# Kernel tuning notes

Hardware: AMD Instinct MI355X
Metric: run time of the kernel (lower is better)

The kernel has to match this reference:

```python
import jax, jax.numpy as jnp
import numpy as np

NUM_HEADS = 8
GROUPS = 8
EPS = 1e-5


def setup_inputs() -> dict:
    key = jax.random.key(0)
    ks = jax.random.split(key, 5)
    B, C, H, W = 2, 512, 64, 64
    x = jax.random.normal(ks[0], (B, C, H, W), dtype=jnp.float32)
    gn_w = jnp.ones((C,), dtype=jnp.float32)
    gn_b = jnp.zeros((C,), dtype=jnp.float32)
    qkv_w = jax.random.normal(ks[1], (3 * C, C), dtype=jnp.float32) * 0.02  # 1x1 conv weight
    qkv_b = jnp.zeros((3 * C,), dtype=jnp.float32)
    proj_w = jax.random.normal(ks[2], (C, C), dtype=jnp.float32) * 0.02
    proj_b = jnp.zeros((C,), dtype=jnp.float32)
    return {"x": x, "gn_w": gn_w, "gn_b": gn_b, "qkv_w": qkv_w,
            "qkv_b": qkv_b, "proj_w": proj_w, "proj_b": proj_b}


def group_norm(x, w, b):
    B, C, H, W = x.shape
    xg = x.reshape(B, GROUPS, C // GROUPS, H, W)
    mean = xg.mean(axis=(2, 3, 4), keepdims=True)
    var = xg.var(axis=(2, 3, 4), keepdims=True)  # biased, matching torch GroupNorm
    h = ((xg - mean) * jax.lax.rsqrt(var + EPS)).reshape(B, C, H, W)
    return h * w[None, :, None, None] + b[None, :, None, None]


def reference(x, gn_w, gn_b, qkv_w, qkv_b, proj_w, proj_b):
    B, C, H, W = x.shape
    nh = NUM_HEADS
    dh = C // nh
    scale = dh ** -0.5
    S = H * W

    h = group_norm(x, gn_w, gn_b)
    # 1x1 conv == per-pixel linear: (B,3C,H,W)
    qkv = jnp.einsum('bchw,oc->bohw', h, qkv_w) + qkv_b[None, :, None, None]
    qkv = qkv.reshape(B, 3, nh, dh, S)
    q = jnp.swapaxes(qkv[:, 0], -1, -2)  # (B, nh, S, dh)
    k = jnp.swapaxes(qkv[:, 1], -1, -2)
    v = jnp.swapaxes(qkv[:, 2], -1, -2)

    attn = jax.nn.softmax(jnp.einsum('bhsd,btd->bhst', q, k.reshape(B * nh, S, dh).reshape(B, nh, S, dh)) * scale, axis=-1) if False else jax.nn.softmax(jnp.einsum('bhsd,bhtd->bhst', q, k) * scale, axis=-1)
    out = jnp.einsum('bhst,bhtd->bhsd', attn, v)  # (B, nh, S, dh)
    out = jnp.swapaxes(out, -1, -2).reshape(B, C, H, W)
    out = jnp.einsum('bchw,oc->bohw', out, proj_w) + proj_b[None, :, None, None]
    return x + out
```

## Files before the change

### kernel.cpp

```cpp
#include <hip/hip_runtime.h>
#include <hip/hip_bf16.h>

typedef __attribute__((ext_vector_type(4)))  float  f32x4;
typedef __attribute__((ext_vector_type(16))) float  f32x16;
typedef __attribute__((ext_vector_type(8)))  short  s16x8;
typedef __attribute__((ext_vector_type(4)))  short  s16x4;
typedef __attribute__((ext_vector_type(4)))  unsigned u32x4;
typedef __attribute__((ext_vector_type(2)))  unsigned u32x2;

__device__ __forceinline__ float bf2f(short v) {
    unsigned u = ((unsigned)(unsigned short)v) << 16;
    return __builtin_bit_cast(float, u);
}
__device__ __forceinline__ short f2bf(float f) {
    unsigned u = __builtin_bit_cast(unsigned, f);
    u += 0x7fff + ((u >> 16) & 1);
    return (short)(u >> 16);
}
__device__ __forceinline__ unsigned cvt_pk_bf16(float lo, float hi) {
    unsigned r;
    asm("v_cvt_pk_bf16_f32 %0, %1, %2" : "=v"(r) : "v"(lo), "v"(hi));
    return r;
}
__device__ __forceinline__ float exp2_asm(float x) {
    float r; asm("v_exp_f32 %0, %1" : "=v"(r) : "v"(x)); return r;
}
__device__ __forceinline__ float log2_asm(float x) {
    float r; asm("v_log_f32 %0, %1" : "=v"(r) : "v"(x)); return r;
}
__device__ __forceinline__ void perm32swap(unsigned &a, unsigned &b) {
    u32x2 r = __builtin_amdgcn_permlane32_swap(a, b, false, false);
    a = r[0]; b = r[1];
}
__device__ __forceinline__ void gload16(const short* g, short* l) {
    __builtin_amdgcn_global_load_lds(
        (const __attribute__((address_space(1))) void*)g,
        (__attribute__((address_space(3))) void*)l, 16, 0, 0);
}

#define BATCH 2
#define CCH   512
#define SSP   4096
#define NH    8
#define DH    64

__global__ __launch_bounds__(256) void wcast_kernel(
    const float* __restrict__ qw, const float* __restrict__ pw,
    short* __restrict__ dq, short* __restrict__ dp)
{
    int idx = (blockIdx.x * 256 + threadIdx.x) * 8;
    const float* src; short* dst;
    if (idx < 786432) { src = qw + idx; dst = dq + idx; }
    else              { src = pw + (idx - 786432); dst = dp + (idx - 786432); }
    f32x4 a = *(const f32x4*)src;
    f32x4 b = *(const f32x4*)(src + 4);
    s16x8 o;
    o[0]=f2bf(a[0]); o[1]=f2bf(a[1]); o[2]=f2bf(a[2]); o[3]=f2bf(a[3]);
    o[4]=f2bf(b[0]); o[5]=f2bf(b[1]); o[6]=f2bf(b[2]); o[7]=f2bf(b[3]);
    *(s16x8*)dst = o;
}

__global__ __launch_bounds__(256) void gn_partial_kernel(
    const float* __restrict__ x, float* __restrict__ part)
{
    int bg = blockIdx.x >> 5, chunk = blockIdx.x & 31;
    const float* base = x + (size_t)bg * 262144 + chunk * 8192;
    int t = threadIdx.x, lane = t & 63, wave = t >> 6;
    float s = 0.f, ss = 0.f;
    #pragma unroll
    for (int k = 0; k < 8; ++k) {
        f32x4 v = *(const f32x4*)&base[k * 1024 + t * 4];
        #pragma unroll
        for (int j = 0; j < 4; ++j) { s += v[j]; ss += v[j] * v[j]; }
    }
    #pragma unroll
    for (int mask = 1; mask < 64; mask <<= 1) {
        s  += __shfl_xor(s,  mask);
        ss += __shfl_xor(ss, mask);
    }
    __shared__ float rs[4], rss[4];
    if (lane == 0) { rs[wave] = s; rss[wave] = ss; }
    __syncthreads();
    if (t == 0) {
        part[blockIdx.x * 2]     = rs[0] + rs[1] + rs[2] + rs[3];
        part[blockIdx.x * 2 + 1] = rss[0] + rss[1] + rss[2] + rss[3];
    }
}

__global__ void gn_final_kernel(const float* __restrict__ part, float* __restrict__ stats)
{
    int t = threadIdx.x;
    if (t < 16) {
        float s = 0.f, ss = 0.f;
        for (int c = 0; c < 32; ++c) {
            s  += part[(t * 32 + c) * 2];
            ss += part[(t * 32 + c) * 2 + 1];
        }
        float mean = s * (1.f / 262144.f);
        float var  = ss * (1.f / 262144.f) - mean * mean;
        stats[t * 2]     = mean;
        stats[t * 2 + 1] = rsqrtf(var + 1e-5f);
    }
}

__global__ __launch_bounds__(256) void gn_apply_kernel(
    const float* __restrict__ x, const float* __restrict__ gw, const float* __restrict__ gb,
    const float* __restrict__ stats, short* __restrict__ hbuf)
{
    __shared__ float tile[64][65];
    int id = blockIdx.x;
    int st = id & 63, ct = (id >> 6) & 7, b = id >> 9;
    int t  = threadIdx.x;
    float mean = stats[(b * 8 + ct) * 2], rstd = stats[(b * 8 + ct) * 2 + 1];
    #pragma unroll
    for (int pass = 0; pass < 4; ++pass) {
        int cr = pass * 16 + (t >> 4);
        int c  = ct * 64 + cr;
        f32x4 v = *(const f32x4*)&x[((size_t)(b * CCH + c)) * SSP + st * 64 + (t & 15) * 4];
        float w  = gw[c] * rstd;
        float bb = gb[c] - mean * w;
        #pragma unroll
        for (int j = 0; j < 4; ++j) tile[cr][(t & 15) * 4 + j] = v[j] * w + bb;
    }
    __syncthreads();
    int sr = t >> 2, cc0 = (t & 3) * 16;
    s16x8 o0, o1;
    #pragma unroll
    for (int j = 0; j < 8; ++j) {
        o0[j] = f2bf(tile[cc0 + j][sr]);
        o1[j] = f2bf(tile[cc0 + 8 + j][sr]);
    }
    short* dst = &hbuf[(size_t)(b * SSP + st * 64 + sr) * CCH + ct * 64 + cc0];
    *(s16x8*)dst = o0;
    *(s16x8*)(dst + 8) = o1;
}

template<int EPI>
__global__ __launch_bounds__(256) void gemm_bt_kernel(
    const short* __restrict__ A, const short* __restrict__ Bt,
    const float* __restrict__ bias,
    short* __restrict__ qout, short* __restrict__ kout, short* __restrict__ vout,
    const float* __restrict__ xres, float* __restrict__ out,
    int K)
{
    __shared__ short As[4096], Bs[4096];
    const int t = threadIdx.x;
    const int lane = t & 63, wave = t >> 6;
    const int wm = wave >> 1, wn = wave & 1;
    const int m0 = blockIdx.x * 128, n0 = blockIdx.y * 128;
    const int l15 = lane & 15, lq = lane >> 4;

    f32x4 acc[4][4];
    #pragma unroll
    for (int i = 0; i < 4; ++i)
        #pragma unroll
        for (int j = 0; j < 4; ++j) acc[i][j] = (f32x4){0.f, 0.f, 0.f, 0.f};

    for (int kk = 0; kk < K; kk += 32) {
        __syncthreads();
        #pragma unroll
        for (int i = 0; i < 2; ++i) {
            int idx = i * 256 + t;
            int row = idx >> 2, cb = idx & 3;
            int dst = ((row >> 4) << 9) + ((((row & 15)) | (cb << 4)) << 3);
            *(s16x8*)&As[dst] = *(const s16x8*)&A [(size_t)(m0 + row) * K + kk + cb * 8];
            *(s16x8*)&Bs[dst] = *(const s16x8*)&Bt[(size_t)(n0 + row) * K + kk + cb * 8];
        }
        __syncthreads();
        s16x8 af[4], bfr[4];
        #pragma unroll
        for (int mt = 0; mt < 4; ++mt) af[mt]  = *(const s16x8*)&As[(((wm * 4 + mt) << 9) + lane * 8)];
        #pragma unroll
        for (int nt = 0; nt < 4; ++nt) bfr[nt] = *(const s16x8*)&Bs[(((wn * 4 + nt) << 9) + lane * 8)];
        #pragma unroll
        for (int mt = 0; mt < 4; ++mt)
            #pragma unroll
            for (int nt = 0; nt < 4; ++nt)
                acc[mt][nt] = __builtin_amdgcn_mfma_f32_16x16x32_bf16(af[mt], bfr[nt], acc[mt][nt], 0, 0, 0);
    }

    #pragma unroll
    for (int mt = 0; mt < 4; ++mt) {
        const int r0 = m0 + wm * 64 + mt * 16 + lq * 4;
        #pragma unroll
        for (int nt = 0; nt < 4; ++nt) {
            const int c = n0 + wn * 64 + nt * 16 + l15;
            float bv = bias[c];
            if (EPI == 0) {
                int bb = r0 >> 12, tloc = r0 & 4095;
                if (c < 512) {
                    #pragma unroll
                    for (int i = 0; i < 4; ++i)
                        qout[(size_t)(r0 + i) * 512 + c] = f2bf(acc[mt][nt][i] + bv);
                } else if (c < 1024) {
                    int hh = (c - 512) >> 6, d = (c - 512) & 63;
                    int T = tloc >> 6, tb = (tloc >> 5) & 1;
                    size_t base = (((size_t)(bb * 8 + hh) * 64 + T) * 8 + tb * 4 + (d >> 4)) * 512
                                  + 256 * ((d >> 3) & 1) + (d & 7);
                    #pragma unroll
                    for (int i = 0; i < 4; ++i)
                        kout[base + ((tloc & 31) + i) * 8] = f2bf(acc[mt][nt][i] + bv);
                } else {
                    int hh = (c - 1024) >> 6, d = (c - 1024) & 63;
                    int T = tloc >> 6, s = (tloc >> 4) & 3, thi = (tloc >> 3) & 1, j0 = tloc & 7;
                    size_t base = (((size_t)(bb * 8 + hh) * 64 + T) * 8 + (d >> 5) * 4 + s) * 512
                                  + ((d & 31) + 32 * thi) * 8 + j0;
                    s16x4 pv;
                    #pragma unroll
                    for (int i = 0; i < 4; ++i) pv[i] = f2bf(acc[mt][nt][i] + bv);
                    *(s16x4*)&vout[base] = pv;
                }
            } else {
                int bb = r0 >> 12, s = r0 & 4095;
                size_t xi = (size_t)(bb * CCH + c) * SSP + s;
                f32x4 xv = *(const f32x4*)&xres[xi];
                f32x4 o  = xv + acc[mt][nt] + bv;
                *(f32x4*)&out[xi] = o;
            }
        }
    }
}

__global__ __launch_bounds__(256, 4) void attn_kernel(
    const short* __restrict__ qbuf, const short* __restrict__ kfrag,
    const short* __restrict__ vfrag,
    short* __restrict__ p0, short* __restrict__ p1, float* __restrict__ aout)
{
    __shared__ short Ks[2][4096];
    __shared__ short Vs[2][4096];
    const int t = threadIdx.x, lane = t & 63, wave = t >> 6;
    const int yy = blockIdx.y, bh = yy & 15, half = yy >> 4;
    const int b = bh >> 3, h = bh & 7;
    const int q0w = blockIdx.x * 128 + wave * 32;
    const int l31 = lane & 31, lh = lane >> 5;
    const int kv0 = half * 2048;

    s16x8 qf[4];
    {
        const short* qp = qbuf + (size_t)(b * SSP + q0w + l31) * 512 + h * 64 + 8 * lh;
        #pragma unroll
        for (int s = 0; s < 4; ++s) {
            s16x8 raw = *(const s16x8*)(qp + 16 * s);
            #pragma unroll
            for (int j = 0; j < 8; ++j) qf[s][j] = f2bf(bf2f(raw[j]) * 0.18033688011112042f);
        }
    }

    const short* kbase = kfrag + (size_t)bh * 262144 + lane * 8;
    const short* vbase = vfrag + (size_t)bh * 262144 + lane * 8;

    f32x16 oacc[2];
    oacc[0] = (f32x16){}; oacc[1] = (f32x16){};
    float m_ = -__builtin_inff(), l_ = 0.f;

    {
        const short* kg = kbase + (size_t)(kv0 >> 6) * 4096 + wave * 1024;
        gload16(kg,       &Ks[0][wave * 1024]);
        gload16(kg + 512, &Ks[0][wave * 1024 + 512]);
        const short* vg = vbase + (size_t)(kv0 >> 6) * 4096 + wave * 1024;
        gload16(vg,       &Vs[0][wave * 1024]);
        gload16(vg + 512, &Vs[0][wave * 1024 + 512]);
    }
    asm volatile("s_waitcnt vmcnt(0)" ::: "memory");
    __syncthreads();

    int cur = 0;
    for (int t0 = kv0; t0 < kv0 + 2048; t0 += 64) {
        if (t0 + 64 < kv0 + 2048) {
            int nb = cur ^ 1;
            const short* kg = kbase + (size_t)((t0 + 64) >> 6) * 4096 + wave * 1024;
            gload16(kg,       &Ks[nb][wave * 1024]);
            gload16(kg + 512, &Ks[nb][wave * 1024 + 512]);
            const short* vg = vbase + (size_t)((t0 + 64) >> 6) * 4096 + wave * 1024;
            gload16(vg,       &Vs[nb][wave * 1024]);
            gload16(vg + 512, &Vs[nb][wave * 1024 + 512]);
        }

        f32x16 sacc[2];
        sacc[0] = (f32x16){}; sacc[1] = (f32x16){};
        __builtin_amdgcn_s_setprio(1);
        #pragma unroll
        for (int s = 0; s < 4; ++s) {
            s16x8 k0 = *(const s16x8*)&Ks[cur][(0 + s) * 512 + lane * 8];
            s16x8 k1 = *(const s16x8*)&Ks[cur][(4 + s) * 512 + lane * 8];
            sacc[0] = __builtin_amdgcn_mfma_f32_32x32x16_bf16(k0, qf[s], sacc[0], 0, 0, 0);
            sacc[1] = __builtin_amdgcn_mfma_f32_32x32x16_bf16(k1, qf[s], sacc[1], 0, 0, 0);
        }
        __builtin_amdgcn_s_setprio(0);

        float mx = sacc[0][0];
        #pragma unroll
        for (int r = 1; r < 16; ++r) mx = fmaxf(mx, sacc[0][r]);
        #pragma unroll
        for (int r = 0; r < 16; ++r) mx = fmaxf(mx, sacc[1][r]);
        int calm = __all(mx <= m_ + 11.5f);
        if (!calm) {
            float g = fmaxf(mx, __shfl_xor(mx, 32));
            float mn = fmaxf(m_, g);
            float corr = exp2_asm(m_ - mn);
            m_ = mn;
            #pragma unroll
            for (int r = 0; r < 16; ++r) { oacc[0][r] *= corr; oacc[1][r] *= corr; }
            l_ *= corr;
        }
        float ts = 0.f;
        #pragma unroll
        for (int tb = 0; tb < 2; ++tb)
            #pragma unroll
            for (int r = 0; r < 16; ++r) {
                float e = exp2_asm(sacc[tb][r] - m_);
                sacc[tb][r] = e;
                ts += e;
            }
        ts += __shfl_xor(ts, 32);
        l_ += ts;

        unsigned w[16];
        #pragma unroll
        for (int tb = 0; tb < 2; ++tb)
            #pragma unroll
            for (int r = 0; r < 8; ++r)
                w[tb * 8 + r] = cvt_pk_bf16(sacc[tb][2 * r], sacc[tb][2 * r + 1]);
        #pragma unroll
        for (int s = 0; s < 4; ++s) {
            perm32swap(w[s * 4 + 0], w[s * 4 + 2]);
            perm32swap(w[s * 4 + 1], w[s * 4 + 3]);
        }

        __builtin_amdgcn_s_setprio(1);
        #pragma unroll
        for (int s = 0; s < 4; ++s) {
            u32x4 pb = { w[s * 4 + 0], w[s * 4 + 1], w[s * 4 + 2], w[s * 4 + 3] };
            s16x8 pB = __builtin_bit_cast(s16x8, pb);
            s16x8 v0 = *(const s16x8*)&Vs[cur][(0 + s) * 512 + lane * 8];
            s16x8 v1 = *(const s16x8*)&Vs[cur][(4 + s) * 512 + lane * 8];
            oacc[0] = __builtin_amdgcn_mfma_f32_32x32x16_bf16(v0, pB, oacc[0], 0, 0, 0);
            oacc[1] = __builtin_amdgcn_mfma_f32_32x32x16_bf16(v1, pB, oacc[1], 0, 0, 0);
        }
        __builtin_amdgcn_s_setprio(0);

        asm volatile("s_waitcnt vmcnt(0)" ::: "memory");
        __syncthreads();
        cur ^= 1;
    }

    short* pO = half ? p1 : p0;
    float linv = 1.f / l_;
    int q = q0w + l31;
    size_t obase = ((size_t)bh * 4096 + q) * 64;
    #pragma unroll
    for (int db = 0; db < 2; ++db)
        #pragma unroll
        for (int g = 0; g < 4; ++g) {
            s16x4 o;
            #pragma unroll
            for (int i = 0; i < 4; ++i) o[i] = f2bf(oacc[db][g * 4 + i] * linv);
            *(s16x4*)&pO[obase + db * 32 + g * 8 + lh * 4] = o;
        }
    if (lh == 0)
        aout[half * 65536 + bh * 4096 + q] = m_ + log2_asm(l_);
}

__global__ __launch_bounds__(256) void combine_kernel(
    const short* __restrict__ p0, const short* __restrict__ p1,
    const float* __restrict__ aout, short* __restrict__ ao)
{
    int bh = blockIdx.x >> 7, q = (blockIdx.x & 127) * 32 + (threadIdx.x >> 3);
    int d0 = (threadIdx.x & 7) * 8;
    size_t pi = ((size_t)bh * 4096 + q) * 64 + d0;
    s16x8 o1 = *(const s16x8*)&p0[pi];
    s16x8 o2 = *(const s16x8*)&p1[pi];
    float a1 = aout[bh * 4096 + q], a2 = aout[65536 + bh * 4096 + q];
    float M = fmaxf(a1, a2);
    float w1 = exp2_asm(a1 - M), w2 = exp2_asm(a2 - M);
    float inv = 1.f / (w1 + w2);
    w1 *= inv; w2 *= inv;
    s16x8 o;
    #pragma unroll
    for (int j = 0; j < 8; ++j) o[j] = f2bf(bf2f(o1[j]) * w1 + bf2f(o2[j]) * w2);
    int b = bh >> 3, h = bh & 7;
    *(s16x8*)&ao[(size_t)(b * SSP + q) * 512 + h * 64 + d0] = o;
}

extern "C" void kernel_launch(void* const* d_in, const int* in_sizes, int n_in,
                              void* d_out, int out_size, void* d_ws, size_t ws_size,
                              hipStream_t stream)
{
    (void)in_sizes; (void)n_in; (void)out_size; (void)ws_size;
    const float* x      = (const float*)d_in[0];
    const float* gn_w   = (const float*)d_in[1];
    const float* gn_b   = (const float*)d_in[2];
    const float* qkv_w  = (const float*)d_in[3];
    const float* qkv_b  = (const float*)d_in[4];
    const float* proj_w = (const float*)d_in[5];
    const float* proj_b = (const float*)d_in[6];
    float* out = (float*)d_out;
    char* ws = (char*)d_ws;

    short* hbuf  = (short*)(ws + 0);
    short* qbuf  = (short*)(ws + 8388608);
    short* kfrag = (short*)(ws + 16777216);
    short* vfrag = (short*)(ws + 25165824);
    short* aobuf = (short*)(ws + 33554432);
    short* wqkv  = (short*)(ws + 41943040);
    short* wproj = (short*)(ws + 43515904);
    float* part  = (float*)(ws + 44040192);
    float* stats = (float*)(ws + 44044288);
    float* ascal = (float*)(ws + 41943040);

    wcast_kernel<<<512, 256, 0, stream>>>(qkv_w, proj_w, wqkv, wproj);
    gn_partial_kernel<<<512, 256, 0, stream>>>(x, part);
    gn_final_kernel<<<1, 64, 0, stream>>>(part, stats);
    gn_apply_kernel<<<1024, 256, 0, stream>>>(x, gn_w, gn_b, stats, hbuf);
    gemm_bt_kernel<0><<<dim3(64, 12), 256, 0, stream>>>(hbuf, wqkv, qkv_b,
                                                        qbuf, kfrag, vfrag, nullptr, nullptr, 512);
    attn_kernel<<<dim3(32, 32), 256, 0, stream>>>(qbuf, kfrag, vfrag,
                                                  hbuf, aobuf, ascal);
    combine_kernel<<<2048, 256, 0, stream>>>(hbuf, aobuf, ascal, kfrag);
    gemm_bt_kernel<1><<<dim3(64, 4), 256, 0, stream>>>(kfrag, wproj, proj_b,
                                                       nullptr, nullptr, nullptr, x, out, 512);
}
```

Before: 158.7 us.

## Double-buffer GEMM tiles via async LDS loads and restructure attention softmax bookkeeping

The GEMM kernel now double-buffers its A/B tiles with global_load_lds, prefetching the next K slice while MFMAs run on the current one. This replaces the synchronous register-staged load followed by two barriers per step. In the attention kernel, the running max is folded into the score accumulator's initial value (nm). The row max uses v_max3 chains, and the row sum is computed by an extra MFMA against a ones vector instead of VALU adds and a shuffle. This trades extra MFMA work and a more intricate numerical path (bf16-rounded probabilities summed, with the max offset baked into the accumulators) for fewer VALU ops and better load/compute overlap.

```diff
diff --git a/kernel.cpp b/kernel.cpp
--- a/kernel.cpp
+++ b/kernel.cpp
@@ -27,6 +27,10 @@
 }
 __device__ __forceinline__ float log2_asm(float x) {
     float r; asm("v_log_f32 %0, %1" : "=v"(r) : "v"(x)); return r;
+}
+__device__ __forceinline__ float max3f(float a, float b, float c) {
+    float r; asm("v_max3_f32 %0, %1, %2, %3" : "=v"(r) : "v"(a), "v"(b), "v"(c));
+    return r;
 }
 __device__ __forceinline__ void perm32swap(unsigned &a, unsigned &b) {
     u32x2 r = __builtin_amdgcn_permlane32_swap(a, b, false, false);
@@ -143,40 +147,57 @@
     const float* __restrict__ xres, float* __restrict__ out,
     int K)
 {
-    __shared__ short As[4096], Bs[4096];
+    __shared__ short As[2][4096], Bs[2][4096];
     const int t = threadIdx.x;
     const int lane = t & 63, wave = t >> 6;
     const int wm = wave >> 1, wn = wave & 1;
     const int m0 = blockIdx.x * 128, n0 = blockIdx.y * 128;
     const int l15 = lane & 15, lq = lane >> 4;
 
+    const int s0r = ((t >> 6) << 4) | (t & 15),          s0c = (t >> 4) & 3;
+    const int s1r = (((256 + t) >> 6) << 4) | (t & 15),  s1c = (t >> 4) & 3;
+    const short* ga0 = A  + (size_t)(m0 + s0r) * K + s0c * 8;
+    const short* ga1 = A  + (size_t)(m0 + s1r) * K + s1c * 8;
+    const short* gb0 = Bt + (size_t)(n0 + s0r) * K + s0c * 8;
+    const short* gb1 = Bt + (size_t)(n0 + s1r) * K + s1c * 8;
+    const int wofs0 = wave * 512;
+    const int wofs1 = 2048 + wave * 512;
+
     f32x4 acc[4][4];
     #pragma unroll
     for (int i = 0; i < 4; ++i)
         #pragma unroll
         for (int j = 0; j < 4; ++j) acc[i][j] = (f32x4){0.f, 0.f, 0.f, 0.f};
 
+    gload16(ga0, &As[0][wofs0]);
+    gload16(ga1, &As[0][wofs1]);
+    gload16(gb0, &Bs[0][wofs0]);
+    gload16(gb1, &Bs[0][wofs1]);
+    asm volatile("s_waitcnt vmcnt(0)" ::: "memory");
+    __syncthreads();
+
+    int cur = 0;
     for (int kk = 0; kk < K; kk += 32) {
-        __syncthreads();
-        #pragma unroll
-        for (int i = 0; i < 2; ++i) {
-            int idx = i * 256 + t;
-            int row = idx >> 2, cb = idx & 3;
-            int dst = ((row >> 4) << 9) + ((((row & 15)) | (cb << 4)) << 3);
-            *(s16x8*)&As[dst] = *(const s16x8*)&A [(size_t)(m0 + row) * K + kk + cb * 8];
-            *(s16x8*)&Bs[dst] = *(const s16x8*)&Bt[(size_t)(n0 + row) * K + kk + cb * 8];
-        }
-        __syncthreads();
+        int nxt = cur ^ 1;
+        if (kk + 32 < K) {
+            gload16(ga0 + kk + 32, &As[nxt][wofs0]);
+            gload16(ga1 + kk + 32, &As[nxt][wofs1]);
+            gload16(gb0 + kk + 32, &Bs[nxt][wofs0]);
+            gload16(gb1 + kk + 32, &Bs[nxt][wofs1]);
+        }
         s16x8 af[4], bfr[4];
         #pragma unroll
-        for (int mt = 0; mt < 4; ++mt) af[mt]  = *(const s16x8*)&As[(((wm * 4 + mt) << 9) + lane * 8)];
-        #pragma unroll
-        for (int nt = 0; nt < 4; ++nt) bfr[nt] = *(const s16x8*)&Bs[(((wn * 4 + nt) << 9) + lane * 8)];
+        for (int mt = 0; mt < 4; ++mt) af[mt]  = *(const s16x8*)&As[cur][((wm * 4 + mt) << 9) + lane * 8];
+        #pragma unroll
+        for (int nt = 0; nt < 4; ++nt) bfr[nt] = *(const s16x8*)&Bs[cur][((wn * 4 + nt) << 9) + lane * 8];
         #pragma unroll
         for (int mt = 0; mt < 4; ++mt)
             #pragma unroll
             for (int nt = 0; nt < 4; ++nt)
                 acc[mt][nt] = __builtin_amdgcn_mfma_f32_16x16x32_bf16(af[mt], bfr[nt], acc[mt][nt], 0, 0, 0);
+        asm volatile("s_waitcnt vmcnt(0)" ::: "memory");
+        __syncthreads();
+        cur = nxt;
     }
 
     #pragma unroll
@@ -251,7 +272,12 @@
 
     f32x16 oacc[2];
     oacc[0] = (f32x16){}; oacc[1] = (f32x16){};
-    float m_ = -__builtin_inff(), l_ = 0.f;
+    f32x16 lacc = (f32x16){};
+    float nm = 0.f;
+
+    s16x8 ones;
+    #pragma unroll
+    for (int j = 0; j < 8; ++j) ones[j] = (short)0x3F80;
 
     {
         const short* kg = kbase + (size_t)(kv0 >> 6) * 4096 + wave * 1024;
@@ -276,51 +302,57 @@
             gload16(vg + 512, &Vs[nb][wave * 1024 + 512]);
         }
 
-        f32x16 sacc[2];
-        sacc[0] = (f32x16){}; sacc[1] = (f32x16){};
+        f32x16 sacc0, sacc1;
+        #pragma unroll
+        for (int r = 0; r < 16; ++r) { sacc0[r] = nm; sacc1[r] = nm; }
         __builtin_amdgcn_s_setprio(1);
         #pragma unroll
         for (int s = 0; s < 4; ++s) {
             s16x8 k0 = *(const s16x8*)&Ks[cur][(0 + s) * 512 + lane * 8];
             s16x8 k1 = *(const s16x8*)&Ks[cur][(4 + s) * 512 + lane * 8];
-            sacc[0] = __builtin_amdgcn_mfma_f32_32x32x16_bf16(k0, qf[s], sacc[0], 0, 0, 0);
-            sacc[1] = __builtin_amdgcn_mfma_f32_32x32x16_bf16(k1, qf[s], sacc[1], 0, 0, 0);
+            sacc0 = __builtin_amdgcn_mfma_f32_32x32x16_bf16(k0, qf[s], sacc0, 0, 0, 0);
+            sacc1 = __builtin_amdgcn_mfma_f32_32x32x16_bf16(k1, qf[s], sacc1, 0, 0, 0);
         }
         __builtin_amdgcn_s_setprio(0);
 
-        float mx = sacc[0][0];
-        #pragma unroll
-        for (int r = 1; r < 16; ++r) mx = fmaxf(mx, sacc[0][r]);
-        #pragma unroll
-        for (int r = 0; r < 16; ++r) mx = fmaxf(mx, sacc[1][r]);
-        int calm = __all(mx <= m_ + 11.5f);
+        float u0 = max3f(sacc0[0],  sacc0[1],  sacc0[2]);
+        float u1 = max3f(sacc0[3],  sacc0[4],  sacc0[5]);
+        float u2 = max3f(sacc0[6],  sacc0[7],  sacc0[8]);
+        float u3 = max3f(sacc0[9],  sacc0[10], sacc0[11]);
+        float u4 = max3f(sacc0[12], sacc0[13], sacc0[14]);
+        float u5 = max3f(sacc1[0],  sacc1[1],  sacc1[2]);
+        float u6 = max3f(sacc1[3],  sacc1[4],  sacc1[5]);
+        float u7 = max3f(sacc1[6],  sacc1[7],  sacc1[8]);
+        float u8 = max3f(sacc1[9],  sacc1[10], sacc1[11]);
+        float u9 = max3f(sacc1[12], sacc1[13], sacc1[14]);
+        float ua = fmaxf(sacc0[15], sacc1[15]);
+        float v0 = max3f(u0, u1, u2);
+        float v1 = max3f(u3, u4, u5);
+        float v2 = max3f(u6, u7, u8);
+        float v3 = max3f(u9, ua, v0);
+        float mx = max3f(v1, v2, v3);
+
+        int calm = __all(mx <= 11.5f);
         if (!calm) {
             float g = fmaxf(mx, __shfl_xor(mx, 32));
-            float mn = fmaxf(m_, g);
-            float corr = exp2_asm(m_ - mn);
-            m_ = mn;
+            float adj = fmaxf(g, 0.f);
+            float corr = exp2_asm(-adj);
+            nm -= adj;
             #pragma unroll
             for (int r = 0; r < 16; ++r) { oacc[0][r] *= corr; oacc[1][r] *= corr; }
-            l_ *= corr;
-        }
-        float ts = 0.f;
-        #pragma unroll
-        for (int tb = 0; tb < 2; ++tb)
+            lacc[0] *= corr;
             #pragma unroll
-            for (int r = 0; r < 16; ++r) {
-                float e = exp2_asm(sacc[tb][r] - m_);
-                sacc[tb][r] = e;
-                ts += e;
-            }
-        ts += __shfl_xor(ts, 32);
-        l_ += ts;
+            for (int r = 0; r < 16; ++r) { sacc0[r] -= adj; sacc1[r] -= adj; }
+        }
+        #pragma unroll
+        for (int r = 0; r < 16; ++r) { sacc0[r] = exp2_asm(sacc0[r]); sacc1[r] = exp2_asm(sacc1[r]); }
 
         unsigned w[16];
         #pragma unroll
-        for (int tb = 0; tb < 2; ++tb)
-            #pragma unroll
-            for (int r = 0; r < 8; ++r)
-                w[tb * 8 + r] = cvt_pk_bf16(sacc[tb][2 * r], sacc[tb][2 * r + 1]);
+        for (int r = 0; r < 8; ++r) {
+            w[r]     = cvt_pk_bf16(sacc0[2 * r], sacc0[2 * r + 1]);
+            w[8 + r] = cvt_pk_bf16(sacc1[2 * r], sacc1[2 * r + 1]);
+        }
         #pragma unroll
         for (int s = 0; s < 4; ++s) {
             perm32swap(w[s * 4 + 0], w[s * 4 + 2]);
@@ -332,10 +364,11 @@
         for (int s = 0; s < 4; ++s) {
             u32x4 pb = { w[s * 4 + 0], w[s * 4 + 1], w[s * 4 + 2], w[s * 4 + 3] };
             s16x8 pB = __builtin_bit_cast(s16x8, pb);
-            s16x8 v0 = *(const s16x8*)&Vs[cur][(0 + s) * 512 + lane * 8];
-            s16x8 v1 = *(const s16x8*)&Vs[cur][(4 + s) * 512 + lane * 8];
-            oacc[0] = __builtin_amdgcn_mfma_f32_32x32x16_bf16(v0, pB, oacc[0], 0, 0, 0);
-            oacc[1] = __builtin_amdgcn_mfma_f32_32x32x16_bf16(v1, pB, oacc[1], 0, 0, 0);
+            s16x8 v0v = *(const s16x8*)&Vs[cur][(0 + s) * 512 + lane * 8];
+            s16x8 v1v = *(const s16x8*)&Vs[cur][(4 + s) * 512 + lane * 8];
+            oacc[0] = __builtin_amdgcn_mfma_f32_32x32x16_bf16(v0v, pB, oacc[0], 0, 0, 0);
+            oacc[1] = __builtin_amdgcn_mfma_f32_32x32x16_bf16(v1v, pB, oacc[1], 0, 0, 0);
+            lacc    = __builtin_amdgcn_mfma_f32_32x32x16_bf16(ones, pB, lacc, 0, 0, 0);
         }
         __builtin_amdgcn_s_setprio(0);
 
@@ -345,6 +378,7 @@
     }
 
     short* pO = half ? p1 : p0;
+    float l_ = lacc[0];
     float linv = 1.f / l_;
     int q = q0w + l31;
     size_t obase = ((size_t)bh * 4096 + q) * 64;
@@ -358,7 +392,7 @@
             *(s16x4*)&pO[obase + db * 32 + g * 8 + lh * 4] = o;
         }
     if (lh == 0)
-        aout[half * 65536 + bh * 4096 + q] = m_ + log2_asm(l_);
+        aout[half * 65536 + bh * 4096 + q] = -nm + log2_asm(l_);
 }
 
 __global__ __launch_bounds__(256) void combine_kernel(
```

Measured after the change: 162.4 us. 2.4% more time.
